# Kernel optimization log

Measured on AMD Instinct MI355X. Metric: run time of the kernel, lower is better.

## Reference

```python
import jax, jax.numpy as jnp
import numpy as np

B, T, DX, DZ, DB, TAU = 256, 1024, 64, 128, 16, 25
CLIP = 10.0


def setup_inputs() -> dict:
    key = jax.random.key(0)
    ks = jax.random.split(key, 16)
    r = lambda k, shape: jax.random.normal(k, shape, jnp.float32)
    u = lambda k, shape, n: jax.random.uniform(k, shape, jnp.float32, -1.0 / np.sqrt(n), 1.0 / np.sqrt(n))
    # AW init (Talathi & Vartak): I + (1/dz) R^T R, scaled to spectral radius 1
    rand = jax.random.normal(ks[0], (DZ, DZ), jnp.float32)
    mat = jnp.eye(DZ, dtype=jnp.float32) + (rand.T @ rand) / DZ
    max_ev = jnp.abs(jnp.linalg.eigvals(mat)).max().real.astype(jnp.float32)
    AW = mat / max_ev
    return {
        "x": r(ks[1], (B, T, DX)),
        "z0": r(ks[2], (B, DZ)),
        "AW": AW,
        "h": u(ks[3], (DZ,), DZ),
        "alphas": u(ks[4], (DB,), DB),
        "thetas": r(ks[5], (DZ, DB)),
        "enc_w1": u(ks[6], (DZ, DX), DX), "enc_b1": u(ks[7], (DZ,), DX),
        "enc_w2": u(ks[8], (DZ, DZ), DZ), "enc_b2": u(ks[9], (DZ,), DZ),
        "dec_w1": u(ks[10], (DZ, DZ), DZ), "dec_b1": u(ks[11], (DZ,), DZ),
        "dec_w2": u(ks[12], (DX, DZ), DZ), "dec_b2": u(ks[13], (DX,), DZ),
    }


def reference(x, z0, AW, h, alphas, thetas,
              enc_w1, enc_b1, enc_w2, enc_b2,
              dec_w1, dec_b1, dec_w2, dec_b2):
    A = jnp.diag(AW)                      # (dz,) diagonal part
    W = AW - jnp.diag(A)                  # (dz,dz) off-diagonal part
    x_t = jnp.swapaxes(x, 0, 1)           # (T,B,dx)
    # encoder applied to all timesteps at once (only used where tf_mask is set)
    enc = jnp.tanh(jnp.tanh(x_t @ enc_w1.T + enc_b1) @ enc_w2.T + enc_b2)  # (T,B,dz)
    t_idx = jnp.arange(T)
    tf_mask = (t_idx % TAU == 0) & (t_idx > 0)   # teacher forcing every tau steps

    def step(z, inp):
        enc_t, m = inp
        z = jnp.where(m, enc_t, z)
        zc = z - z.mean(axis=1, keepdims=True)   # mean-centering norm
        # basis expansion: sum_d alphas[d] * relu(zc + thetas[:,d])  -> (B,dz)
        basis = jnp.einsum('bkd,d->bk', jax.nn.relu(zc[:, :, None] + thetas), alphas)
        z_next = A * z + basis @ W.T + h
        z_next = jnp.clip(z_next, -CLIP, CLIP)
        return z_next, z_next

    _, z_seq = jax.lax.scan(step, z0, (enc, tf_mask))     # (T,B,dz)
    x_pred = jnp.tanh(jnp.tanh(z_seq @ dec_w1.T + dec_b1) @ dec_w2.T + dec_b2)  # (T,B,dx)
    return jnp.swapaxes(x_pred, 0, 1), jnp.swapaxes(z_seq, 0, 1)
```

## Files before the change

kernel.cpp:

```cpp
#include <hip/hip_runtime.h>
#include <hip/hip_bf16.h>

constexpr int BB  = 256;
constexpr int TT  = 1024;
constexpr int DXc = 64;
constexpr int DZc = 128;
constexpr int DBc = 16;
constexpr int TAUc = 25;
constexpr float CLIPV = 10.0f;
constexpr int NF = 40;
constexpr int NSEG = 41;
constexpr int GRP = 16;

typedef __attribute__((ext_vector_type(8))) short short8;
typedef __attribute__((ext_vector_type(8))) _Float16 half8;
typedef __attribute__((ext_vector_type(4))) float f32x4;
typedef __attribute__((ext_vector_type(4))) unsigned u32x4;
typedef __attribute__((ext_vector_type(2))) unsigned u32x2;

__device__ __forceinline__ unsigned perm_b32(unsigned a, unsigned b, unsigned s) {
  return __builtin_amdgcn_perm(a, b, s);
}

__device__ __forceinline__ void pack_hilo8(const f32x4 a, const f32x4 b,
                                           short8& hi, short8& lo) {
  float f[8];
  *(f32x4*)&f[0] = a;
  *(f32x4*)&f[4] = b;
  u32x4 hi4, lo4;
  #pragma unroll
  for (int p = 0; p < 4; ++p) {
    const unsigned b0 = __float_as_uint(f[2 * p]);
    const unsigned b1 = __float_as_uint(f[2 * p + 1]);
    hi4[p] = perm_b32(b1, b0, 0x07060302u);
    const float l0 = f[2 * p]     - __uint_as_float(b0 & 0xFFFF0000u);
    const float l1 = f[2 * p + 1] - __uint_as_float(b1 & 0xFFFF0000u);
    lo4[p] = perm_b32(__float_as_uint(l1), __float_as_uint(l0), 0x07060302u);
  }
  hi = __builtin_bit_cast(short8, hi4);
  lo = __builtin_bit_cast(short8, lo4);
}

__device__ __forceinline__ half8 cvt8_f16(const f32x4 a, const f32x4 b) {
  float f[8];
  *(f32x4*)&f[0] = a;
  *(f32x4*)&f[4] = b;
  u32x4 h4;
  #pragma unroll
  for (int p = 0; p < 4; ++p) {
    const _Float16 h0 = (_Float16)f[2 * p], h1 = (_Float16)f[2 * p + 1];
    h4[p] = (unsigned)__builtin_bit_cast(unsigned short, h0)
          | ((unsigned)__builtin_bit_cast(unsigned short, h1) << 16);
  }
  return __builtin_bit_cast(half8, h4);
}

__device__ __forceinline__ void cvt8_f16_hilo(const f32x4 a, const f32x4 b,
                                              half8& hi, half8& lo) {
  float f[8];
  *(f32x4*)&f[0] = a;
  *(f32x4*)&f[4] = b;
  u32x4 h4, l4;
  #pragma unroll
  for (int p = 0; p < 4; ++p) {
    const float f0 = f[2 * p], f1 = f[2 * p + 1];
    const _Float16 h0 = (_Float16)f0, h1 = (_Float16)f1;
    const float r0 = f0 - (float)h0, r1 = f1 - (float)h1;
    const _Float16 e0 = (_Float16)r0, e1 = (_Float16)r1;
    h4[p] = (unsigned)__builtin_bit_cast(unsigned short, h0)
          | ((unsigned)__builtin_bit_cast(unsigned short, h1) << 16);
    l4[p] = (unsigned)__builtin_bit_cast(unsigned short, e0)
          | ((unsigned)__builtin_bit_cast(unsigned short, e1) << 16);
  }
  hi = __builtin_bit_cast(half8, h4);
  lo = __builtin_bit_cast(half8, l4);
}

__device__ __forceinline__ unsigned pk2_f16(float a, float b) {
  const _Float16 ha = (_Float16)a, hb = (_Float16)b;
  return (unsigned)__builtin_bit_cast(unsigned short, ha)
       | ((unsigned)__builtin_bit_cast(unsigned short, hb) << 16);
}

__device__ __forceinline__ void pk4_f16_hilo(const f32x4 v, u32x2& hi, u32x2& lo) {
  const _Float16 h0 = (_Float16)v[0], h1 = (_Float16)v[1];
  const _Float16 h2 = (_Float16)v[2], h3 = (_Float16)v[3];
  const float r0 = v[0] - (float)h0, r1 = v[1] - (float)h1;
  const float r2 = v[2] - (float)h2, r3 = v[3] - (float)h3;
  hi[0] = (unsigned)__builtin_bit_cast(unsigned short, h0)
        | ((unsigned)__builtin_bit_cast(unsigned short, h1) << 16);
  hi[1] = (unsigned)__builtin_bit_cast(unsigned short, h2)
        | ((unsigned)__builtin_bit_cast(unsigned short, h3) << 16);
  lo[0] = pk2_f16(r0, r1);
  lo[1] = pk2_f16(r2, r3);
}

__device__ __forceinline__ float ftanh(float x) {
  const float ax = __builtin_fabsf(x);
  const float p  = __builtin_amdgcn_exp2f(ax * 2.8853900817779268f);
  const float r  = __builtin_amdgcn_rcpf(p + 1.0f);
  const float t  = __builtin_fmaf(-2.0f, r, 1.0f);
  return __builtin_copysignf(t, x);
}

#define SCAN_BAR() do { \
    __asm__ volatile("s_waitcnt lgkmcnt(0)" ::: "memory"); \
    __builtin_amdgcn_s_barrier(); \
    __asm__ volatile("" ::: "memory"); } while (0)

constexpr int ENC_NT = 4;

__global__ __launch_bounds__(256, 2) void enc_mfma_kernel(
    const float* __restrict__ x, const float* __restrict__ w1,
    const float* __restrict__ b1v, const float* __restrict__ w2,
    const float* __restrict__ b2v, float* __restrict__ zs)
{
  const int tid = threadIdx.x;
  const int w = tid >> 6, l = tid & 63;
  const int rowf = l & 15;
  const int kg = l >> 4;

  __shared__ unsigned hb[2][16][68];

  half8 W1f[2][2], W2f[2][4];
  #pragma unroll
  for (int tm = 0; tm < 2; ++tm) {
    const int m = (2 * w + tm) * 16 + rowf;
    #pragma unroll
    for (int kt = 0; kt < 2; ++kt) {
      const int k0 = kt * 32 + kg * 8;
      W1f[tm][kt] = cvt8_f16(*(const f32x4*)&w1[m * DXc + k0],
                             *(const f32x4*)&w1[m * DXc + k0 + 4]);
    }
    #pragma unroll
    for (int kt = 0; kt < 4; ++kt) {
      const int k0 = kt * 32 + kg * 8;
      W2f[tm][kt] = cvt8_f16(*(const f32x4*)&w2[m * DZc + k0],
                             *(const f32x4*)&w2[m * DZc + k0 + 4]);
    }
  }
  float b1r[2][4], b2r[2][4];
  #pragma unroll
  for (int tm = 0; tm < 2; ++tm)
    #pragma unroll
    for (int j = 0; j < 4; ++j) {
      b1r[tm][j] = b1v[(2 * w + tm) * 16 + kg * 4 + j];
      b2r[tm][j] = b2v[(2 * w + tm) * 16 + kg * 4 + j];
    }

  for (int it = 0; it < ENC_NT; ++it) {
    const int r = blockIdx.x * (ENC_NT * 16) + it * 16 + rowf;
    const int f = r >> 8, b = r & 255;
    const int t = TAUc * (f + 1);
    const float* xr = x + ((size_t)b * TT + t) * DXc + kg * 8;

    f32x4 aH0 = {b1r[0][0], b1r[0][1], b1r[0][2], b1r[0][3]};
    f32x4 aH1 = {b1r[1][0], b1r[1][1], b1r[1][2], b1r[1][3]};
    f32x4 aL0 = {0.f, 0.f, 0.f, 0.f}, aL1 = {0.f, 0.f, 0.f, 0.f};
    #pragma unroll
    for (int kt = 0; kt < 2; ++kt) {
      half8 xh, xl;
      cvt8_f16_hilo(*(const f32x4*)&xr[kt * 32], *(const f32x4*)&xr[kt * 32 + 4],
                    xh, xl);
      aH0 = __builtin_amdgcn_mfma_f32_16x16x32_f16(W1f[0][kt], xh, aH0, 0, 0, 0);
      aH1 = __builtin_amdgcn_mfma_f32_16x16x32_f16(W1f[1][kt], xh, aH1, 0, 0, 0);
      aL0 = __builtin_amdgcn_mfma_f32_16x16x32_f16(W1f[0][kt], xl, aL0, 0, 0, 0);
      aL1 = __builtin_amdgcn_mfma_f32_16x16x32_f16(W1f[1][kt], xl, aL1, 0, 0, 0);
    }
    {
      u32x2 pk0, pk1;
      pk0[0] = pk2_f16(ftanh(aH0[0] + aL0[0]), ftanh(aH0[1] + aL0[1]));
      pk0[1] = pk2_f16(ftanh(aH0[2] + aL0[2]), ftanh(aH0[3] + aL0[3]));
      pk1[0] = pk2_f16(ftanh(aH1[0] + aL1[0]), ftanh(aH1[1] + aL1[1]));
      pk1[1] = pk2_f16(ftanh(aH1[2] + aL1[2]), ftanh(aH1[3] + aL1[3]));
      *(u32x2*)&hb[it & 1][rowf][(2 * w + 0) * 8 + kg * 2] = pk0;
      *(u32x2*)&hb[it & 1][rowf][(2 * w + 1) * 8 + kg * 2] = pk1;
    }
    SCAN_BAR();

    #pragma unroll
    for (int tm = 0; tm < 2; ++tm) {
      f32x4 a2 = {b2r[tm][0], b2r[tm][1], b2r[tm][2], b2r[tm][3]};
      #pragma unroll
      for (int kt = 0; kt < 4; ++kt) {
        const u32x4 hp = *(const u32x4*)&hb[it & 1][rowf][kt * 16 + kg * 4];
        a2 = __builtin_amdgcn_mfma_f32_16x16x32_f16(W2f[tm][kt],
                 __builtin_bit_cast(half8, hp), a2, 0, 0, 0);
      }
      f32x4 ov;
      #pragma unroll
      for (int j = 0; j < 4; ++j) ov[j] = ftanh(a2[j]);
      *(f32x4*)&zs[((size_t)b * TT + t) * DZc + (2 * w + tm) * 16 + kg * 4] = ov;
    }
  }
}

__global__ __launch_bounds__(256, 1) void scan_dec_kernel(
    const float* __restrict__ AW, const float* __restrict__ z0,
    const float* __restrict__ hvec, const float* __restrict__ alphas,
    const float* __restrict__ thetas,
    const float* __restrict__ dw1, const float* __restrict__ db1,
    const float* __restrict__ dw2, const float* __restrict__ db2,
    float* __restrict__ zs, float* __restrict__ xp)
{
  const int bid = blockIdx.x;
  const int g = bid & 15;
  const int s = bid >> 4;
  const int t0 = s * TAUc;
  const int nsteps = (s == NSEG - 1) ? (TT - t0) : TAUc;

  const int tid = threadIdx.x;
  const int w = tid >> 6, l = tid & 63;
  const int rowf = l & 15;
  const int kg = l >> 4;

  __shared__ float zbuf[DZc][20];
  __shared__ float meanp[16][4];
  __shared__ unsigned pbuf[16][DZc + 4];
  __shared__ unsigned zpkh[16][68];
  __shared__ unsigned zpkl[16][68];
  __shared__ unsigned hbuf[16][68];

  short8 Whi[2][4], Wlo[2][4];
  #pragma unroll
  for (int tm = 0; tm < 2; ++tm) {
    const int m = (2 * w + tm) * 16 + rowf;
    #pragma unroll
    for (int kt = 0; kt < 4; ++kt) {
      const int kb = kt * 32 + kg * 8;
      float f[8];
      #pragma unroll
      for (int i = 0; i < 8; ++i) {
        const int k = kb + i;
        f[i] = (k == m) ? 0.f : AW[m * DZc + k];
      }
      pack_hilo8(*(const f32x4*)&f[0], *(const f32x4*)&f[4],
                 Whi[tm][kt], Wlo[tm][kt]);
    }
  }
  float a_d[2][4], h_d[2][4];
  #pragma unroll
  for (int tm = 0; tm < 2; ++tm)
    #pragma unroll
    for (int j = 0; j < 4; ++j) {
      const int comp = (2 * w + tm) * 16 + kg * 4 + j;
      a_d[tm][j] = AW[comp * DZc + comp];
      h_d[tm][j] = hvec[comp];
    }

  half8 D1f[2][4], D2f[4];
  #pragma unroll
  for (int tm = 0; tm < 2; ++tm) {
    const int m = (2 * w + tm) * 16 + rowf;
    #pragma unroll
    for (int kt = 0; kt < 4; ++kt) {
      const int k0 = kt * 32 + kg * 8;
      D1f[tm][kt] = cvt8_f16(*(const f32x4*)&dw1[m * DZc + k0],
                             *(const f32x4*)&dw1[m * DZc + k0 + 4]);
    }
  }
  {
    const int m2 = w * 16 + rowf;
    #pragma unroll
    for (int kt = 0; kt < 4; ++kt) {
      const int k0 = kt * 32 + kg * 8;
      D2f[kt] = cvt8_f16(*(const f32x4*)&dw2[m2 * DZc + k0],
                         *(const f32x4*)&dw2[m2 * DZc + k0 + 4]);
    }
  }
  float d1b[2][4], d2b[4];
  #pragma unroll
  for (int tm = 0; tm < 2; ++tm)
    #pragma unroll
    for (int j = 0; j < 4; ++j)
      d1b[tm][j] = db1[(2 * w + tm) * 16 + kg * 4 + j];
  #pragma unroll
  for (int j = 0; j < 4; ++j)
    d2b[j] = db2[w * 16 + kg * 4 + j];

  const int cb = tid >> 1;
  const int rh = tid & 1;
  float th[DBc], al[DBc];
  #pragma unroll
  for (int d = 0; d < DBc; ++d) {
    th[d] = thetas[cb * DBc + d];
    al[d] = alphas[d];
  }

  const int brow = g * GRP + rowf;
  const size_t zb_row = (size_t)brow * TT * DZc;
  const size_t xp_row = (size_t)brow * TT * DXc;
  f32x4 z[2];
  #pragma unroll
  for (int tm = 0; tm < 2; ++tm) {
    const int comp0 = (2 * w + tm) * 16 + kg * 4;
    if (s == 0) z[tm] = *(const f32x4*)&z0[brow * DZc + comp0];
    else        z[tm] = *(const f32x4*)&zs[zb_row + (size_t)t0 * DZc + comp0];
  }

#define PUB_ZPK() do { \
    _Pragma("unroll") \
    for (int tm = 0; tm < 2; ++tm) { \
      u32x2 zh_, zl_; \
      pk4_f16_hilo(z[tm], zh_, zl_); \
      *(u32x2*)&zpkh[rowf][(2 * w + tm) * 8 + kg * 2] = zh_; \
      *(u32x2*)&zpkl[rowf][(2 * w + tm) * 8 + kg * 2] = zl_; \
    } } while (0)

#define DEC_L1() do { \
    f32x4 dAh = {d1b[0][0], d1b[0][1], d1b[0][2], d1b[0][3]}; \
    f32x4 dBh = {d1b[1][0], d1b[1][1], d1b[1][2], d1b[1][3]}; \
    f32x4 dAl = {0.f, 0.f, 0.f, 0.f}, dBl = {0.f, 0.f, 0.f, 0.f}; \
    _Pragma("unroll") \
    for (int kt = 0; kt < 4; ++kt) { \
      const u32x4 bh = *(const u32x4*)&zpkh[rowf][kt * 16 + kg * 4]; \
      const u32x4 bl = *(const u32x4*)&zpkl[rowf][kt * 16 + kg * 4]; \
      const half8 Bh = __builtin_bit_cast(half8, bh); \
      const half8 Bl = __builtin_bit_cast(half8, bl); \
      dAh = __builtin_amdgcn_mfma_f32_16x16x32_f16(D1f[0][kt], Bh, dAh, 0, 0, 0); \
      dBh = __builtin_amdgcn_mfma_f32_16x16x32_f16(D1f[1][kt], Bh, dBh, 0, 0, 0); \
      dAl = __builtin_amdgcn_mfma_f32_16x16x32_f16(D1f[0][kt], Bl, dAl, 0, 0, 0); \
      dBl = __builtin_amdgcn_mfma_f32_16x16x32_f16(D1f[1][kt], Bl, dBl, 0, 0, 0); \
    } \
    u32x2 pk0, pk1; \
    pk0[0] = pk2_f16(ftanh(dAh[0] + dAl[0]), ftanh(dAh[1] + dAl[1])); \
    pk0[1] = pk2_f16(ftanh(dAh[2] + dAl[2]), ftanh(dAh[3] + dAl[3])); \
    pk1[0] = pk2_f16(ftanh(dBh[0] + dBl[0]), ftanh(dBh[1] + dBl[1])); \
    pk1[1] = pk2_f16(ftanh(dBh[2] + dBl[2]), ftanh(dBh[3] + dBl[3])); \
    *(u32x2*)&hbuf[rowf][(2 * w + 0) * 8 + kg * 2] = pk0; \
    *(u32x2*)&hbuf[rowf][(2 * w + 1) * 8 + kg * 2] = pk1; \
    } while (0)

#define DEC_L2(TD) do { \
    f32x4 a2 = {d2b[0], d2b[1], d2b[2], d2b[3]}; \
    _Pragma("unroll") \
    for (int kt = 0; kt < 4; ++kt) { \
      const u32x4 hp = *(const u32x4*)&hbuf[rowf][kt * 16 + kg * 4]; \
      a2 = __builtin_amdgcn_mfma_f32_16x16x32_f16(D2f[kt], \
               __builtin_bit_cast(half8, hp), a2, 0, 0, 0); \
    } \
    f32x4 ov; \
    _Pragma("unroll") \
    for (int j = 0; j < 4; ++j) ov[j] = ftanh(a2[j]); \
    *(f32x4*)&xp[xp_row + (size_t)(TD) * DXc + w * 16 + kg * 4] = ov; \
    } while (0)

  for (int it = 0; it < nsteps; ++it) {
    const int t = t0 + it;

    float ssum = ((z[0][0] + z[0][1]) + (z[0][2] + z[0][3]))
               + ((z[1][0] + z[1][1]) + (z[1][2] + z[1][3]));
    ssum += __shfl_xor(ssum, 16, 64);
    ssum += __shfl_xor(ssum, 32, 64);
    if (l < 16) meanp[l][w] = ssum;
    #pragma unroll
    for (int tm = 0; tm < 2; ++tm)
      #pragma unroll
      for (int j = 0; j < 4; ++j)
        zbuf[(2 * w + tm) * 16 + kg * 4 + j][rowf] = z[tm][j];
    PUB_ZPK();
    SCAN_BAR();

    {
      float zr[8], mean[8];
      *(f32x4*)&zr[0] = *(const f32x4*)&zbuf[cb][rh * 8];
      *(f32x4*)&zr[4] = *(const f32x4*)&zbuf[cb][rh * 8 + 4];
      #pragma unroll
      for (int q = 0; q < 8; ++q) {
        const f32x4 mp = *(const f32x4*)&meanp[rh * 8 + q][0];
        mean[q] = ((mp[0] + mp[1]) + (mp[2] + mp[3])) * (1.0f / 128.0f);
      }
      #pragma unroll
      for (int q = 0; q < 8; ++q) {
        const float zc = zr[q] - mean[q];
        float bs = 0.f;
        #pragma unroll
        for (int d = 0; d < DBc; ++d)
          bs = fmaf(al[d], fmaxf(zc + th[d], 0.f), bs);
        const unsigned fb = __float_as_uint(bs);
        const float lof = bs - __uint_as_float(fb & 0xFFFF0000u);
        const unsigned pk = perm_b32(__float_as_uint(lof), fb, 0x07060302u);
        pbuf[rh * 8 + q][cb] = pk;
      }
    }
    if (it > 0) DEC_L1();
    SCAN_BAR();

    if (it > 0) DEC_L2(t - 1);
    {
      f32x4 acc1[2], acc2[2];
      #pragma unroll
      for (int tm = 0; tm < 2; ++tm)
        #pragma unroll
        for (int j = 0; j < 4; ++j) {
          acc1[tm][j] = fmaf(a_d[tm][j], z[tm][j], h_d[tm][j]);
          acc2[tm][j] = 0.f;
        }
      #pragma unroll
      for (int kt = 0; kt < 4; ++kt) {
        const int cbase = kt * 32 + kg * 8;
        const u32x4 p0 = *(const u32x4*)&pbuf[rowf][cbase];
        const u32x4 p1 = *(const u32x4*)&pbuf[rowf][cbase + 4];
        u32x4 hi4, lo4;
        hi4[0] = perm_b32(p0[1], p0[0], 0x05040100u);
        hi4[1] = perm_b32(p0[3], p0[2], 0x05040100u);
        hi4[2] = perm_b32(p1[1], p1[0], 0x05040100u);
        hi4[3] = perm_b32(p1[3], p1[2], 0x05040100u);
        lo4[0] = perm_b32(p0[1], p0[0], 0x07060302u);
        lo4[1] = perm_b32(p0[3], p0[2], 0x07060302u);
        lo4[2] = perm_b32(p1[1], p1[0], 0x07060302u);
        lo4[3] = perm_b32(p1[3], p1[2], 0x07060302u);
        const short8 Bhi = __builtin_bit_cast(short8, hi4);
        const short8 Blo = __builtin_bit_cast(short8, lo4);
        acc1[0] = __builtin_amdgcn_mfma_f32_16x16x32_bf16(Whi[0][kt], Bhi, acc1[0], 0, 0, 0);
        acc1[1] = __builtin_amdgcn_mfma_f32_16x16x32_bf16(Whi[1][kt], Bhi, acc1[1], 0, 0, 0);
        acc2[0] = __builtin_amdgcn_mfma_f32_16x16x32_bf16(Whi[0][kt], Blo, acc2[0], 0, 0, 0);
        acc2[0] = __builtin_amdgcn_mfma_f32_16x16x32_bf16(Wlo[0][kt], Bhi, acc2[0], 0, 0, 0);
        acc2[1] = __builtin_amdgcn_mfma_f32_16x16x32_bf16(Whi[1][kt], Blo, acc2[1], 0, 0, 0);
        acc2[1] = __builtin_amdgcn_mfma_f32_16x16x32_bf16(Wlo[1][kt], Bhi, acc2[1], 0, 0, 0);
      }
      #pragma unroll
      for (int tm = 0; tm < 2; ++tm) {
        f32x4 zn;
        #pragma unroll
        for (int j = 0; j < 4; ++j) {
          float v = acc1[tm][j] + acc2[tm][j];
          zn[j] = fminf(fmaxf(v, -CLIPV), CLIPV);
        }
        *(f32x4*)&zs[zb_row + (size_t)t * DZc + (2 * w + tm) * 16 + kg * 4] = zn;
        z[tm] = zn;
      }
    }
  }

  PUB_ZPK();
  SCAN_BAR();
  DEC_L1();
  SCAN_BAR();
  DEC_L2(t0 + nsteps - 1);

#undef PUB_ZPK
#undef DEC_L1
#undef DEC_L2
}

extern "C" void kernel_launch(void* const* d_in, const int* in_sizes, int n_in,
                              void* d_out, int out_size, void* d_ws, size_t ws_size,
                              hipStream_t stream) {
  const float* x      = (const float*)d_in[0];
  const float* z0     = (const float*)d_in[1];
  const float* AW     = (const float*)d_in[2];
  const float* hvec   = (const float*)d_in[3];
  const float* alphas = (const float*)d_in[4];
  const float* thetas = (const float*)d_in[5];
  const float* ew1    = (const float*)d_in[6];
  const float* eb1    = (const float*)d_in[7];
  const float* ew2    = (const float*)d_in[8];
  const float* eb2    = (const float*)d_in[9];
  const float* dw1    = (const float*)d_in[10];
  const float* db1    = (const float*)d_in[11];
  const float* dw2    = (const float*)d_in[12];
  const float* db2    = (const float*)d_in[13];

  float* xp = (float*)d_out;
  float* zs = xp + (size_t)BB * TT * DXc;

  hipLaunchKernelGGL(enc_mfma_kernel,
                     dim3(NF * BB / (ENC_NT * 16)), dim3(256), 0, stream,
                     x, ew1, eb1, ew2, eb2, zs);

  hipLaunchKernelGGL(scan_dec_kernel, dim3((BB / GRP) * NSEG), dim3(256), 0, stream,
                     AW, z0, hvec, alphas, thetas, dw1, db1, dw2, db2, zs, xp);
}
```

Measured before the change: 156.2 us.

## Pre-split basis into hi/lo bf16 LDS planes, move decoder layer earlier, add priorities

The basis stage now has each thread handle two adjacent z components for four batch rows. It packs the bf16 hi parts and the residual lo parts directly into separate LDS arrays, so the MFMA stage reads B operands with plain vector loads and no per-step perm shuffles. DEC_L1 moves ahead of the basis computation, and s_setprio raises wave priority around it and the MFMA loop to favour the latency-critical recurrence. alphas are loaded as scalars via readfirstlane. This adds LDS traffic with two arrays and changes register pressure from the doubled theta arrays.

```diff
diff --git a/kernel.cpp b/kernel.cpp
--- a/kernel.cpp
+++ b/kernel.cpp
@@ -101,6 +101,10 @@
   const float r  = __builtin_amdgcn_rcpf(p + 1.0f);
   const float t  = __builtin_fmaf(-2.0f, r, 1.0f);
   return __builtin_copysignf(t, x);
+}
+
+__device__ __forceinline__ float sload(const float* p) {
+  return __uint_as_float(__builtin_amdgcn_readfirstlane(__float_as_uint(*p)));
 }
 
 #define SCAN_BAR() do { \
@@ -216,7 +220,8 @@
 
   __shared__ float zbuf[DZc][20];
   __shared__ float meanp[16][4];
-  __shared__ unsigned pbuf[16][DZc + 4];
+  __shared__ unsigned pbh[16][68];
+  __shared__ unsigned pbl[16][68];
   __shared__ unsigned zpkh[16][68];
   __shared__ unsigned zpkl[16][68];
   __shared__ unsigned hbuf[16][68];
@@ -278,13 +283,14 @@
   for (int j = 0; j < 4; ++j)
     d2b[j] = db2[w * 16 + kg * 4 + j];
 
-  const int cb = tid >> 1;
-  const int rh = tid & 1;
-  float th[DBc], al[DBc];
+  const int pb = tid >> 2;
+  const int rq = tid & 3;
+  float th0[DBc], th1[DBc], al[DBc];
   #pragma unroll
   for (int d = 0; d < DBc; ++d) {
-    th[d] = thetas[cb * DBc + d];
-    al[d] = alphas[d];
+    th0[d] = thetas[(2 * pb) * DBc + d];
+    th1[d] = thetas[(2 * pb + 1) * DBc + d];
+    al[d]  = sload(&alphas[d]);
   }
 
   const int brow = g * GRP + rowf;
@@ -361,29 +367,42 @@
     PUB_ZPK();
     SCAN_BAR();
 
+    if (it > 0) {
+      __builtin_amdgcn_s_setprio(1);
+      DEC_L1();
+      __builtin_amdgcn_s_setprio(0);
+    }
     {
-      float zr[8], mean[8];
-      *(f32x4*)&zr[0] = *(const f32x4*)&zbuf[cb][rh * 8];
-      *(f32x4*)&zr[4] = *(const f32x4*)&zbuf[cb][rh * 8 + 4];
-      #pragma unroll
-      for (int q = 0; q < 8; ++q) {
-        const f32x4 mp = *(const f32x4*)&meanp[rh * 8 + q][0];
-        mean[q] = ((mp[0] + mp[1]) + (mp[2] + mp[3])) * (1.0f / 128.0f);
-      }
-      #pragma unroll
-      for (int q = 0; q < 8; ++q) {
-        const float zc = zr[q] - mean[q];
-        float bs = 0.f;
+      float z0r[4], z1r[4], mean[4];
+      *(f32x4*)&z0r[0] = *(const f32x4*)&zbuf[2 * pb][rq * 4];
+      *(f32x4*)&z1r[0] = *(const f32x4*)&zbuf[2 * pb + 1][rq * 4];
+      #pragma unroll
+      for (int j = 0; j < 4; ++j) {
+        const f32x4 mp = *(const f32x4*)&meanp[rq * 4 + j][0];
+        mean[j] = ((mp[0] + mp[1]) + (mp[2] + mp[3])) * (1.0f / 128.0f);
+      }
+      #pragma unroll
+      for (int j = 0; j < 4; ++j) {
+        const float zc0 = z0r[j] - mean[j];
+        const float zc1 = z1r[j] - mean[j];
+        float b0 = 0.f, b1 = 0.f;
         #pragma unroll
-        for (int d = 0; d < DBc; ++d)
-          bs = fmaf(al[d], fmaxf(zc + th[d], 0.f), bs);
-        const unsigned fb = __float_as_uint(bs);
-        const float lof = bs - __uint_as_float(fb & 0xFFFF0000u);
-        const unsigned pk = perm_b32(__float_as_uint(lof), fb, 0x07060302u);
-        pbuf[rh * 8 + q][cb] = pk;
-      }
-    }
-    if (it > 0) DEC_L1();
+        for (int d = 0; d < DBc; ++d) {
+          b0 = fmaf(al[d], fmaxf(zc0 + th0[d], 0.f), b0);
+          b1 = fmaf(al[d], fmaxf(zc1 + th1[d], 0.f), b1);
+        }
+        const unsigned u0 = __float_as_uint(b0);
+        const unsigned u1 = __float_as_uint(b1);
+        const unsigned hiw = perm_b32(u1, u0, 0x07060302u);
+        const float l0 = b0 - __uint_as_float(u0 & 0xFFFF0000u);
+        const float l1 = b1 - __uint_as_float(u1 & 0xFFFF0000u);
+        const unsigned low = perm_b32(__float_as_uint(l1), __float_as_uint(l0),
+                                      0x07060302u);
+        const int r = rq * 4 + j;
+        pbh[r][pb] = hiw;
+        pbl[r][pb] = low;
+      }
+    }
     SCAN_BAR();
 
     if (it > 0) DEC_L2(t - 1);
@@ -396,22 +415,13 @@
           acc1[tm][j] = fmaf(a_d[tm][j], z[tm][j], h_d[tm][j]);
           acc2[tm][j] = 0.f;
         }
+      __builtin_amdgcn_s_setprio(1);
       #pragma unroll
       for (int kt = 0; kt < 4; ++kt) {
-        const int cbase = kt * 32 + kg * 8;
-        const u32x4 p0 = *(const u32x4*)&pbuf[rowf][cbase];
-        const u32x4 p1 = *(const u32x4*)&pbuf[rowf][cbase + 4];
-        u32x4 hi4, lo4;
-        hi4[0] = perm_b32(p0[1], p0[0], 0x05040100u);
-        hi4[1] = perm_b32(p0[3], p0[2], 0x05040100u);
-        hi4[2] = perm_b32(p1[1], p1[0], 0x05040100u);
-        hi4[3] = perm_b32(p1[3], p1[2], 0x05040100u);
-        lo4[0] = perm_b32(p0[1], p0[0], 0x07060302u);
-        lo4[1] = perm_b32(p0[3], p0[2], 0x07060302u);
-        lo4[2] = perm_b32(p1[1], p1[0], 0x07060302u);
-        lo4[3] = perm_b32(p1[3], p1[2], 0x07060302u);
-        const short8 Bhi = __builtin_bit_cast(short8, hi4);
-        const short8 Blo = __builtin_bit_cast(short8, lo4);
+        const u32x4 bh = *(const u32x4*)&pbh[rowf][kt * 16 + kg * 4];
+        const u32x4 bl = *(const u32x4*)&pbl[rowf][kt * 16 + kg * 4];
+        const short8 Bhi = __builtin_bit_cast(short8, bh);
+        const short8 Blo = __builtin_bit_cast(short8, bl);
         acc1[0] = __builtin_amdgcn_mfma_f32_16x16x32_bf16(Whi[0][kt], Bhi, acc1[0], 0, 0, 0);
         acc1[1] = __builtin_amdgcn_mfma_f32_16x16x32_bf16(Whi[1][kt], Bhi, acc1[1], 0, 0, 0);
         acc2[0] = __builtin_amdgcn_mfma_f32_16x16x32_bf16(Whi[0][kt], Blo, acc2[0], 0, 0, 0);
@@ -419,6 +429,7 @@
         acc2[1] = __builtin_amdgcn_mfma_f32_16x16x32_bf16(Whi[1][kt], Blo, acc2[1], 0, 0, 0);
         acc2[1] = __builtin_amdgcn_mfma_f32_16x16x32_bf16(Wlo[1][kt], Bhi, acc2[1], 0, 0, 0);
       }
+      __builtin_amdgcn_s_setprio(0);
       #pragma unroll
       for (int tm = 0; tm < 2; ++tm) {
         f32x4 zn;
```

New measurement: 207.6 us. 32.9% more time.
